# Kernel tuning notes

Measured on AMD Instinct MI355X. Metric: run time of the kernel, lower is better.

The kernel has to match this reference:

```python
import jax, jax.numpy as jnp
import numpy as np

N_NODES = 8192
N_EDGES = 65536
D_MODEL = 64
D_INNER = 128
D_STATE = 16
DT_RANK = 4
LAYER_NUM = 3
TAU = 0.01


def _unif(key, shape, fan_out):
    stdv = 1.0 / np.sqrt(fan_out)
    return jax.random.uniform(key, shape, jnp.float32, -stdv, stdv)


def setup_inputs() -> dict:
    key = jax.random.key(0)
    ks = jax.random.split(key, 12)
    x = jax.random.normal(ks[0], (N_NODES, D_MODEL), jnp.float32)
    edge_index = jax.random.randint(ks[1], (2, N_EDGES), 0, N_NODES, jnp.int64)
    in_proj_w = _unif(ks[2], (D_MODEL, 2 * D_INNER), 2 * D_INNER)
    x_proj_w = _unif(ks[3], (D_INNER, DT_RANK + 2 * D_STATE), DT_RANK + 2 * D_STATE)
    dt_proj_w = _unif(ks[4], (DT_RANK, D_INNER), D_INNER)
    out_proj_w = _unif(ks[5], (D_INNER, D_MODEL), D_MODEL)
    A_log = jnp.log(jnp.broadcast_to(jnp.arange(1, D_STATE + 1, dtype=jnp.float32)[None, :], (D_INNER, D_STATE)))
    D = jnp.ones((D_INNER,), jnp.float32)
    in_act_w = _unif(ks[6], (D_INNER, 2), 2)
    in_act_b = _unif(ks[7], (2,), 2)
    out_act_w = _unif(ks[8], (D_INNER, 2), 2)
    out_act_b = _unif(ks[9], (2,), 2)
    return {"x": x, "in_proj_w": in_proj_w, "x_proj_w": x_proj_w, "dt_proj_w": dt_proj_w,
            "A_log": A_log, "D": D, "out_proj_w": out_proj_w,
            "in_act_w": in_act_w, "in_act_b": in_act_b, "out_act_w": out_act_w, "out_act_b": out_act_b,
            "edge_index": edge_index, "layer_num": LAYER_NUM}


def _norm_adj(row, col, w, n_nodes):
    # SparseTensor(...).set_diag() adds diag value 1; symmetric deg^-1/2 renorm
    deg = jax.ops.segment_sum(w, row, num_segments=n_nodes) + 1.0
    dinv = jnp.where(deg > 0, deg ** -0.5, 0.0)
    return dinv[row] * w * dinv[col], dinv * dinv  # off-diag edge weights, diag weights


def _spmm(row, col, ew, dw, x, n_nodes):
    # adj @ x with adj = edges(ew) + diag(dw); x: [N, F]
    return jax.ops.segment_sum(ew[:, None] * x[col], row, num_segments=n_nodes) + dw[:, None] * x


def _gumbel_hard(logits, key, tau):
    g = jax.random.gumbel(key, logits.shape, logits.dtype)
    y = jax.nn.softmax((logits + g) / tau, axis=-1)
    hard = jax.nn.one_hot(jnp.argmax(y, axis=-1), logits.shape[-1], dtype=y.dtype)
    return hard + y - jax.lax.stop_gradient(y)


def reference(x, in_proj_w, x_proj_w, dt_proj_w, A_log, D, out_proj_w,
              in_act_w, in_act_b, out_act_w, out_act_b, edge_index, layer_num):
    n_nodes, d_model = x.shape
    d_inner = dt_proj_w.shape[1]
    n = A_log.shape[1]
    dt_rank = dt_proj_w.shape[0]
    row, col = edge_index[0], edge_index[1]

    xl = jnp.broadcast_to(x[:, None, :], (n_nodes, layer_num, d_model))  # [N,L,d_model]
    x_and_res = xl @ in_proj_w                                           # [N,L,2*d_inner]
    xs, res = jnp.split(x_and_res, 2, axis=-1)
    xs = jax.nn.relu(xs)                                                 # u in scan

    A = -jnp.exp(A_log)                                                  # [d_inner, n]
    x_dbl = xs @ x_proj_w                                                # [N,L,dt_rank+2n]
    delta = jax.nn.softplus(x_dbl[..., :dt_rank] @ dt_proj_w)            # [N,L,d_inner]
    B = x_dbl[..., dt_rank:dt_rank + n]                                  # [N,L,n]
    C = x_dbl[..., dt_rank + n:]                                         # [N,L,n]

    deltaA = jnp.exp(jnp.einsum('bld,dn->bldn', delta, A))               # [N,L,d_inner,n]
    deltaB_u = jnp.einsum('bld,bln->bldn', delta * xs, B)                # [N,L,d_inner,n]

    # initial adjacency: unit-weight edges, sym-normalized with self loops
    ew, dw = _norm_adj(row, col, jnp.ones((row.shape[0],), xs.dtype), n_nodes)
    state = jnp.zeros((n_nodes, d_inner, n), xs.dtype)
    gkey = jax.random.key(42)
    ys = []
    for i in range(layer_num):  # small fixed number of GCN/SSM steps
        state = deltaA[:, i] * state + deltaB_u[:, i]
        y = jnp.einsum('bdn,bn->bd', state, C[:, i])                     # [N,d_inner]
        flat = _spmm(row, col, ew, dw, state.reshape(n_nodes, d_inner * n), n_nodes)
        state = flat.reshape(n_nodes, d_inner, n)
        in_p = _gumbel_hard(y @ in_act_w + in_act_b, jax.random.fold_in(gkey, 2 * i), TAU)
        out_p = _gumbel_hard(y @ out_act_w + out_act_b, jax.random.fold_in(gkey, 2 * i + 1), TAU)
        w = in_p[col, 0] * out_p[row, 0]  # keep_in_prob[v] * keep_out_prob[u]
        ew, dw = _norm_adj(row, col, w, n_nodes)
        ys.append(y)

    y = jnp.stack(ys, axis=1) + xs * D                                   # [N,L,d_inner]
    y = y * jax.nn.relu(res)
    out = y @ out_proj_w                                                 # [N,L,d_model]
    return out[:, -1, :]
```

## Files before the change

kernel.cpp:

```cpp
#include <hip/hip_runtime.h>
#include <cstdint>

#define NN 8192
#define NE 65536
#define G 8
#define CAP 64

typedef _Float16 h8 __attribute__((ext_vector_type(8)));
typedef _Float16 h2 __attribute__((ext_vector_type(2)));

__device__ inline int rdlane_i(int v, int l) {
  return __builtin_amdgcn_readlane(v, l);
}
__device__ inline float rdlane_f(float v, int l) {
  return __int_as_float(__builtin_amdgcn_readlane(__float_as_int(v), l));
}

__host__ __device__ inline void tf2x32(uint32_t k0, uint32_t k1,
                                       uint32_t x0, uint32_t x1,
                                       uint32_t& r0, uint32_t& r1) {
  uint32_t ks2 = k0 ^ k1 ^ 0x1BD11BDAu;
  x0 += k0; x1 += k1;
#define TF_ROT(x,d) (((x)<<(d))|((x)>>(32-(d))))
#define TF_R4(ra,rb,rc,rd) \
  x0+=x1; x1=TF_ROT(x1,ra); x1^=x0; \
  x0+=x1; x1=TF_ROT(x1,rb); x1^=x0; \
  x0+=x1; x1=TF_ROT(x1,rc); x1^=x0; \
  x0+=x1; x1=TF_ROT(x1,rd); x1^=x0;
  TF_R4(13,15,26,6)  x0+=k1;  x1+=ks2+1u;
  TF_R4(17,29,16,24) x0+=ks2; x1+=k0+2u;
  TF_R4(13,15,26,6)  x0+=k0;  x1+=k1+3u;
  TF_R4(17,29,16,24) x0+=k1;  x1+=ks2+4u;
  TF_R4(13,15,26,6)  x0+=ks2; x1+=k0+5u;
  r0=x0; r1=x1;
#undef TF_R4
#undef TF_ROT
}

__device__ inline float gumbel32(uint32_t k0, uint32_t k1, uint32_t idx) {
  uint32_t a, b;
  tf2x32(k0, k1, 0u, idx, a, b);
  uint32_t bits = a ^ b;
  float f = __uint_as_float((bits >> 9) | 0x3f800000u) - 1.0f;
  float u = (f > 0.0f) ? f : 1.17549435e-38f;
  return -logf(-logf(u));
}

__global__ __launch_bounds__(256) void k_nodeprep(
    const float* __restrict__ x, const float* __restrict__ ipw,
    const float* __restrict__ xpw, const float* __restrict__ dtw,
    const float* __restrict__ iaw, const float* __restrict__ iab,
    const float* __restrict__ oaw, const float* __restrict__ oab,
    const float* __restrict__ alog, const float* __restrict__ wout,
    const int* __restrict__ ei,
    uint32_t ki0, uint32_t ki1, uint32_t ko0, uint32_t ko1,
    float* __restrict__ xs, float* __restrict__ rres,
    float* __restrict__ delta, _Float16* __restrict__ dxh2,
    float* __restrict__ Bm, float* __restrict__ Cm,
    float* __restrict__ inp, float* __restrict__ outp,
    float* __restrict__ Amat, _Float16* __restrict__ woT,
    int* __restrict__ cnt, int* __restrict__ csr_col) {
  __shared__ float sxs[G][128];
  __shared__ float sdbl[G][36];
  __shared__ float sdx[G][128];
  int t = threadIdx.x;
  int b0 = blockIdx.x * G;
  if (t < 64) {
    int e = blockIdx.x * 64 + t;
    int v = ei[e];
    int pos = atomicAdd(&cnt[v], 1);
    if (pos < CAP) csr_col[(v<<6) + pos] = ei[NE + e];
  }
  {
    int i = blockIdx.x * 8 + (t & 7);
    if (t < 8) {
      int d = i >> 6, oc = i & 63;
      woT[oc*128 + d] = (_Float16)wout[i];
    }
  }
  if (blockIdx.x == 0) {
    for (int i = t; i < 2048; i += 256) Amat[i] = -expf(alog[i]);
  }
  float acc[G];
#pragma unroll
  for (int g = 0; g < G; g++) acc[g] = 0.f;
  const float4* xb = (const float4*)(x + (size_t)b0 * 64);
  for (int k4 = 0; k4 < 16; k4++) {
    float w0 = ipw[(k4*4+0)*256 + t];
    float w1 = ipw[(k4*4+1)*256 + t];
    float w2 = ipw[(k4*4+2)*256 + t];
    float w3 = ipw[(k4*4+3)*256 + t];
#pragma unroll
    for (int g = 0; g < G; g++) {
      float4 xv = xb[g*16 + k4];
      acc[g] += xv.x*w0; acc[g] += xv.y*w1; acc[g] += xv.z*w2; acc[g] += xv.w*w3;
    }
  }
  if (t < 128) {
#pragma unroll
    for (int g = 0; g < G; g++) {
      float v = fmaxf(acc[g], 0.f);
      sxs[g][t] = v;
      xs[(size_t)(b0+g)*128 + t] = v;
    }
  } else {
    int j = t - 128;
#pragma unroll
    for (int g = 0; g < G; g++) rres[(size_t)(b0+g)*128 + j] = fmaxf(acc[g], 0.f);
  }
  __syncthreads();
  for (int idx = t; idx < G*36; idx += 256) {
    int g = idx / 36, c = idx % 36;
    float a = 0.f;
    for (int d4 = 0; d4 < 32; d4++) {
      float4 sv = ((const float4*)&sxs[g][0])[d4];
      a += sv.x*xpw[(d4*4+0)*36 + c];
      a += sv.y*xpw[(d4*4+1)*36 + c];
      a += sv.z*xpw[(d4*4+2)*36 + c];
      a += sv.w*xpw[(d4*4+3)*36 + c];
    }
    sdbl[g][c] = a;
    if (c >= 4 && c < 20)  Bm[(b0+g)*16 + (c-4)]  = a;
    else if (c >= 20)      Cm[(b0+g)*16 + (c-20)] = a;
  }
  __syncthreads();
  {
    int d = t & 127, hi = t >> 7;
#pragma unroll
    for (int gg = 0; gg < G/2; gg++) {
      int g = hi*(G/2) + gg;
      int b = b0 + g;
      float dt = sdbl[g][0]*dtw[d]     + sdbl[g][1]*dtw[128+d]
               + sdbl[g][2]*dtw[256+d] + sdbl[g][3]*dtw[384+d];
      float dv = fmaxf(dt, 0.f) + log1pf(expf(-fabsf(dt)));
      delta[(size_t)b*128 + d] = dv;
      sdx[g][d] = dv * sxs[g][d];
    }
  }
  __syncthreads();
  for (int i = t; i < G*64; i += 256) {
    int g = i >> 6, d = i & 63;
    h2 pk;
    pk.x = (_Float16)sdx[g][d];
    pk.y = (_Float16)sdx[g][d + 64];
    ((h2*)(dxh2 + ((size_t)(b0+g) << 7)))[d] = pk;
  }
  int wid = t >> 6, lane = t & 63;
#pragma unroll
  for (int s = 0; s < 2; s++) {
    int g = wid*2 + s;
    int b = b0 + g;
    float da = sdx[g][lane], db = sdx[g][lane + 64];
    float4 pr;
    pr.x = da*iaw[2*lane]   + db*iaw[2*(lane+64)];
    pr.y = da*iaw[2*lane+1] + db*iaw[2*(lane+64)+1];
    pr.z = da*oaw[2*lane]   + db*oaw[2*(lane+64)];
    pr.w = da*oaw[2*lane+1] + db*oaw[2*(lane+64)+1];
    for (int off = 32; off >= 1; off >>= 1) {
      pr.x += __shfl_down(pr.x, off);
      pr.y += __shfl_down(pr.y, off);
      pr.z += __shfl_down(pr.z, off);
      pr.w += __shfl_down(pr.w, off);
    }
    float gsel = 0.f;
    if (lane < 4) {
      uint32_t kk0 = (lane < 2) ? ki0 : ko0;
      uint32_t kk1 = (lane < 2) ? ki1 : ko1;
      gsel = gumbel32(kk0, kk1, 2u*(uint32_t)b + (uint32_t)(lane & 1));
    }
    float g0 = __shfl(gsel, 0), g1 = __shfl(gsel, 1);
    float g2 = __shfl(gsel, 2), g3 = __shfl(gsel, 3);
    if (lane == 0) {
      float BC = 0.f;
      for (int n = 0; n < 16; n++) BC += sdbl[g][4+n] * sdbl[g][20+n];
      float li0 = BC*pr.x + iab[0], li1 = BC*pr.y + iab[1];
      float lo0 = BC*pr.z + oab[0], lo1 = BC*pr.w + oab[1];
      inp[b]  = (li0 + g0 >= li1 + g1) ? 1.0f : 0.0f;
      outp[b] = (lo0 + g2 >= lo1 + g3) ? 1.0f : 0.0f;
    }
  }
}

__global__ __launch_bounds__(256) void k_spmm0f(
    const int* __restrict__ cnt, const int* __restrict__ csr_col,
    const float* __restrict__ inp, const float* __restrict__ outp,
    const float* __restrict__ delta, const _Float16* __restrict__ dxh2,
    const float* __restrict__ Bm, const float* __restrict__ Cm,
    const float* __restrict__ Amat,
    _Float16* __restrict__ s_out, float* __restrict__ dinv1,
    float* __restrict__ y2p) {
  int t = threadIdx.x, wid = t >> 6, lane = t & 63;
  int v = (blockIdx.x << 2) + wid;
  int deg = min(cnt[v], CAP);
  int   creg = 0;
  float cfreg = 0.f, gl = 0.f;
  if (lane < deg) {
    creg = csr_col[(v << 6) + lane];
    cfreg = 1.0f / sqrtf((float)min(cnt[creg], CAP) + 1.0f);
    gl = inp[creg];
  }
  float degs = gl;
#pragma unroll
  for (int off = 32; off >= 1; off >>= 1) degs += __shfl_xor(degs, off);
  int d0 = lane, d1 = lane + 64;
  float dv = 1.0f / sqrtf((float)deg + 1.0f);
  h2 pkv = ((const h2*)(dxh2 + ((size_t)v << 7)))[d0];
  float dx0 = (float)pkv.x, dx1 = (float)pkv.y;
  float Bf[16];
  {
    const float4* p = (const float4*)(Bm + ((size_t)v << 4));
    float4 q0 = p[0], q1 = p[1], q2 = p[2], q3 = p[3];
    Bf[0]=q0.x; Bf[1]=q0.y; Bf[2]=q0.z; Bf[3]=q0.w;
    Bf[4]=q1.x; Bf[5]=q1.y; Bf[6]=q1.z; Bf[7]=q1.w;
    Bf[8]=q2.x; Bf[9]=q2.y; Bf[10]=q2.z; Bf[11]=q2.w;
    Bf[12]=q3.x; Bf[13]=q3.y; Bf[14]=q3.z; Bf[15]=q3.w;
  }
  float a0[16], a1[16];
  {
    float dw = dv * dv;
    float c0 = dw * dx0, c1 = dw * dx1;
#pragma unroll
    for (int n = 0; n < 16; n++) { a0[n] = c0*Bf[n]; a1[n] = c1*Bf[n]; }
  }
#pragma unroll 2
  for (int j = 0; j < deg; j++) {
    int   c  = rdlane_i(creg, j);
    float cf = rdlane_f(cfreg, j);
    float coef = dv * cf;
    h2 pk = ((const h2*)(dxh2 + ((size_t)c << 7)))[d0];
    const float4* bp = (const float4*)(Bm + ((size_t)c << 4));
    float4 B0 = bp[0], B1 = bp[1], B2 = bp[2], B3 = bp[3];
    float e0 = coef * (float)pk.x;
    float e1 = coef * (float)pk.y;
    a0[0]+=e0*B0.x; a0[1]+=e0*B0.y; a0[2]+=e0*B0.z; a0[3]+=e0*B0.w;
    a0[4]+=e0*B1.x; a0[5]+=e0*B1.y; a0[6]+=e0*B1.z; a0[7]+=e0*B1.w;
    a0[8]+=e0*B2.x; a0[9]+=e0*B2.y; a0[10]+=e0*B2.z; a0[11]+=e0*B2.w;
    a0[12]+=e0*B3.x; a0[13]+=e0*B3.y; a0[14]+=e0*B3.z; a0[15]+=e0*B3.w;
    a1[0]+=e1*B0.x; a1[1]+=e1*B0.y; a1[2]+=e1*B0.z; a1[3]+=e1*B0.w;
    a1[4]+=e1*B1.x; a1[5]+=e1*B1.y; a1[6]+=e1*B1.z; a1[7]+=e1*B1.w;
    a1[8]+=e1*B2.x; a1[9]+=e1*B2.y; a1[10]+=e1*B2.z; a1[11]+=e1*B2.w;
    a1[12]+=e1*B3.x; a1[13]+=e1*B3.y; a1[14]+=e1*B3.z; a1[15]+=e1*B3.w;
  }
  float de0 = delta[(size_t)v*128 + d0], de1 = delta[(size_t)v*128 + d1];
  const float4* A0p = (const float4*)(Amat + (d0 << 4));
  const float4* A1p = (const float4*)(Amat + (d1 << 4));
  const float4* Cp  = (const float4*)(Cm + ((size_t)v << 4));
  float d1v = 1.0f / sqrtf(outp[v]*degs + 1.0f);
  if (lane == 0) dinv1[v] = d1v;
  float dw1 = d1v * d1v;
  float y0 = 0.f, y1 = 0.f, BvC = 0.f;
  _Float16 sh0[16], sh1[16];
#pragma unroll
  for (int q = 0; q < 4; q++) {
    float4 Aq0 = A0p[q], Aq1 = A1p[q], Cq = Cp[q];
    float A0a[4] = {Aq0.x, Aq0.y, Aq0.z, Aq0.w};
    float A1a[4] = {Aq1.x, Aq1.y, Aq1.z, Aq1.w};
    float Ca[4]  = {Cq.x, Cq.y, Cq.z, Cq.w};
#pragma unroll
    for (int i = 0; i < 4; i++) {
      int n = 4*q + i;
      float E0 = expf(de0 * A0a[i]);
      float E1 = expf(de1 * A1a[i]);
      float s0 = E0*a0[n] + dx0*Bf[n];
      float s1 = E1*a1[n] + dx1*Bf[n];
      y0 += E0*s0*Ca[i];
      y1 += E1*s1*Ca[i];
      BvC += Bf[n]*Ca[i];
      sh0[n] = (_Float16)s0;
      sh1[n] = (_Float16)s1;
    }
  }
  y0 = dw1*y0 + dx0*BvC;
  y1 = dw1*y1 + dx1*BvC;
  if (inp[v] != 0.f) {
    h8 P00, P01, P10, P11;
#pragma unroll
    for (int i = 0; i < 8; i++) {
      P00[i] = sh0[i]; P01[i] = sh0[8+i];
      P10[i] = sh1[i]; P11[i] = sh1[8+i];
    }
    h8* op = (h8*)(s_out + ((size_t)v << 11));
    op[2*lane]           = P00;
    op[2*lane + 1]       = P01;
    op[128 + 2*lane]     = P10;
    op[128 + 2*lane + 1] = P11;
  }
  y2p[(size_t)v*128 + d0] = y0;
  y2p[(size_t)v*128 + d1] = y1;
}

__global__ __launch_bounds__(256) void k_spmm1fo(
    const int* __restrict__ cnt, const int* __restrict__ csr_col,
    const float* __restrict__ dinv1,
    const float* __restrict__ inp, const float* __restrict__ outp,
    const float* __restrict__ delta,
    const float* __restrict__ Cm, const float* __restrict__ Amat,
    const _Float16* __restrict__ s_in, const float* __restrict__ y2p,
    const float* __restrict__ xs, const float* __restrict__ rres,
    const float* __restrict__ Dv, const _Float16* __restrict__ woT,
    float* __restrict__ out) {
  __shared__ float ty[4][128];
  int t = threadIdx.x, wid = t >> 6, lane = t & 63;
  int v = (blockIdx.x << 2) + wid;
  int deg = (outp[v] != 0.f) ? min(cnt[v], CAP) : 0;
  int   creg = 0;
  float cfreg = 0.f;
  if (lane < deg) {
    creg = csr_col[(v << 6) + lane];
    float g = inp[creg];
    cfreg = (g != 0.f) ? dinv1[creg] : 0.f;
  }
  unsigned long long mask = __ballot(cfreg != 0.f);
  int d0 = lane, d1 = lane + 64;
  float y0 = 0.f, y1 = 0.f;
  if (mask != 0ull) {
    float dv = dinv1[v];
    float a0[16], a1[16];
#pragma unroll
    for (int n = 0; n < 16; n++) { a0[n] = 0.f; a1[n] = 0.f; }
#pragma unroll 2
    for (int j = 0; j < deg; j++) {
      float cf = rdlane_f(cfreg, j);
      if (cf == 0.f) continue;
      int c = rdlane_i(creg, j);
      float coef = dv * cf;
      const h8* rp = (const h8*)(s_in + ((size_t)c << 11));
      h8 n00 = rp[2*lane], n01 = rp[2*lane+1];
      h8 n10 = rp[128 + 2*lane], n11 = rp[128 + 2*lane+1];
      a0[0]+=coef*(float)n00[0]; a0[1]+=coef*(float)n00[1];
      a0[2]+=coef*(float)n00[2]; a0[3]+=coef*(float)n00[3];
      a0[4]+=coef*(float)n00[4]; a0[5]+=coef*(float)n00[5];
      a0[6]+=coef*(float)n00[6]; a0[7]+=coef*(float)n00[7];
      a0[8]+=coef*(float)n01[0]; a0[9]+=coef*(float)n01[1];
      a0[10]+=coef*(float)n01[2]; a0[11]+=coef*(float)n01[3];
      a0[12]+=coef*(float)n01[4]; a0[13]+=coef*(float)n01[5];
      a0[14]+=coef*(float)n01[6]; a0[15]+=coef*(float)n01[7];
      a1[0]+=coef*(float)n10[0]; a1[1]+=coef*(float)n10[1];
      a1[2]+=coef*(float)n10[2]; a1[3]+=coef*(float)n10[3];
      a1[4]+=coef*(float)n10[4]; a1[5]+=coef*(float)n10[5];
      a1[6]+=coef*(float)n10[6]; a1[7]+=coef*(float)n10[7];
      a1[8]+=coef*(float)n11[0]; a1[9]+=coef*(float)n11[1];
      a1[10]+=coef*(float)n11[2]; a1[11]+=coef*(float)n11[3];
      a1[12]+=coef*(float)n11[4]; a1[13]+=coef*(float)n11[5];
      a1[14]+=coef*(float)n11[6]; a1[15]+=coef*(float)n11[7];
    }
    float de0 = delta[(size_t)v*128 + d0], de1 = delta[(size_t)v*128 + d1];
    const float4* A0p = (const float4*)(Amat + (d0 << 4));
    const float4* A1p = (const float4*)(Amat + (d1 << 4));
    const float4* Cp  = (const float4*)(Cm + ((size_t)v << 4));
#pragma unroll
    for (int q = 0; q < 4; q++) {
      float4 Aq0 = A0p[q], Aq1 = A1p[q], Cq = Cp[q];
      float A0a[4] = {Aq0.x, Aq0.y, Aq0.z, Aq0.w};
      float A1a[4] = {Aq1.x, Aq1.y, Aq1.z, Aq1.w};
      float Ca[4]  = {Cq.x, Cq.y, Cq.z, Cq.w};
#pragma unroll
      for (int i = 0; i < 4; i++) {
        int n = 4*q + i;
        y0 += expf(de0*A0a[i]) * a0[n] * Ca[i];
        y1 += expf(de1*A1a[i]) * a1[n] * Ca[i];
      }
    }
  }
  float t0 = (y0 + y2p[(size_t)v*128 + d0] + xs[(size_t)v*128 + d0]*Dv[d0]) * rres[(size_t)v*128 + d0];
  float t1 = (y1 + y2p[(size_t)v*128 + d1] + xs[(size_t)v*128 + d1]*Dv[d1]) * rres[(size_t)v*128 + d1];
  ty[wid][d0] = t0;
  ty[wid][d1] = t1;
  asm volatile("s_waitcnt lgkmcnt(0)" ::: "memory");
  __builtin_amdgcn_sched_barrier(0);
  float acc = 0.f;
  const float4* tyv = (const float4*)&ty[wid][0];
  const h8* wrow = (const h8*)(woT + ((size_t)lane << 7));
#pragma unroll
  for (int ch = 0; ch < 16; ch++) {
    h8 wv = wrow[ch];
    float4 u0 = tyv[2*ch], u1 = tyv[2*ch+1];
    acc += u0.x*(float)wv[0] + u0.y*(float)wv[1] + u0.z*(float)wv[2] + u0.w*(float)wv[3]
         + u1.x*(float)wv[4] + u1.y*(float)wv[5] + u1.z*(float)wv[6] + u1.w*(float)wv[7];
  }
  out[(size_t)v*64 + lane] = acc;
}

extern "C" void kernel_launch(void* const* d_in, const int* in_sizes, int n_in,
                              void* d_out, int out_size, void* d_ws, size_t ws_size,
                              hipStream_t stream) {
  const float* x    = (const float*)d_in[0];
  const float* ipw  = (const float*)d_in[1];
  const float* xpw  = (const float*)d_in[2];
  const float* dtw  = (const float*)d_in[3];
  const float* alog = (const float*)d_in[4];
  const float* Dv   = (const float*)d_in[5];
  const float* wout = (const float*)d_in[6];
  const float* iaw  = (const float*)d_in[7];
  const float* iab  = (const float*)d_in[8];
  const float* oaw  = (const float*)d_in[9];
  const float* oab  = (const float*)d_in[10];
  const int*   ei   = (const int*)d_in[11];
  (void)in_sizes; (void)n_in; (void)out_size; (void)ws_size;

  float* W = (float*)d_ws;
  size_t o = 0;
  float* xs    = W + o; o += (size_t)NN*128;
  float* rres  = W + o; o += (size_t)NN*128;
  float* delta = W + o; o += (size_t)NN*128;
  float* y2p   = W + o; o += (size_t)NN*128;
  float* Bm    = W + o; o += (size_t)NN*16;
  float* Cm    = W + o; o += (size_t)NN*16;
  float* Amat  = W + o; o += 2048;
  float* dinv1 = W + o; o += NN;
  float* inp   = W + o; o += NN;
  float* outp  = W + o; o += NN;
  _Float16* dxh2 = (_Float16*)(W + o); o += (size_t)NN*64;
  o += (size_t)NN*8;
  _Float16* woT  = (_Float16*)(W + o); o += 4096;
  _Float16* stA  = (_Float16*)(W + o); o += (size_t)NN*1024;
  int* cnt     = (int*)(W + o);
  int* csr_col = cnt + NN;

  uint32_t ki0, ki1, ko0, ko1;
  tf2x32(0u, 42u, 0u, 0u, ki0, ki1);
  tf2x32(0u, 42u, 0u, 1u, ko0, ko1);

  hipMemsetAsync(cnt, 0, NN*sizeof(int), stream);

  k_nodeprep<<<NN/G, 256, 0, stream>>>(x, ipw, xpw, dtw, iaw, iab, oaw, oab,
                                       alog, wout, ei, ki0, ki1, ko0, ko1,
                                       xs, rres, delta, dxh2, Bm, Cm,
                                       inp, outp, Amat, woT, cnt, csr_col);

  k_spmm0f<<<NN/4, 256, 0, stream>>>(cnt, csr_col, inp, outp,
                                     delta, dxh2, Bm, Cm, Amat,
                                     stA, dinv1, y2p);

  k_spmm1fo<<<NN/4, 256, 0, stream>>>(cnt, csr_col, dinv1, inp, outp,
                                      delta, Cm, Amat, stA, y2p,
                                      xs, rres, Dv, woT, (float*)d_out);
}
```

Before: 160.3 us.

## Split each node's d_inner channels across two waves in both SpMM kernels

Both SpMM kernels now assign one node to two waves, each wave handling 64 of the 128 inner channels, instead of one wave covering all 128. This halves the per-thread accumulator registers and doubles the number of waves, which is meant to raise occupancy and latency hiding for the gather-bound loops. The output projection is split by channel halves and combined through shared memory with block-wide barriers. The cost is duplicated neighbour-list loads, reductions and B-row reads per node, plus the added synchronisation.

```diff
diff --git a/kernel.cpp b/kernel.cpp
--- a/kernel.cpp
+++ b/kernel.cpp
@@ -189,9 +189,13 @@
     const float* __restrict__ Amat,
     _Float16* __restrict__ s_out, float* __restrict__ dinv1,
     float* __restrict__ y2p) {
-  int t = threadIdx.x, wid = t >> 6, lane = t & 63;
-  int v = (blockIdx.x << 2) + wid;
+  int t = threadIdx.x, wave = t >> 6, lane = t & 63;
+  int v = (blockIdx.x << 1) + (wave >> 1);
+  int w = wave & 1;
+  int d = (w << 6) + lane;
   int deg = min(cnt[v], CAP);
+  float inpv = inp[v];
+  float outpv = outp[v];
   int   creg = 0;
   float cfreg = 0.f, gl = 0.f;
   if (lane < deg) {
@@ -202,10 +206,9 @@
   float degs = gl;
 #pragma unroll
   for (int off = 32; off >= 1; off >>= 1) degs += __shfl_xor(degs, off);
-  int d0 = lane, d1 = lane + 64;
   float dv = 1.0f / sqrtf((float)deg + 1.0f);
-  h2 pkv = ((const h2*)(dxh2 + ((size_t)v << 7)))[d0];
-  float dx0 = (float)pkv.x, dx1 = (float)pkv.y;
+  h2 pkv = ((const h2*)(dxh2 + ((size_t)v << 7)))[lane];
+  float dx = w ? (float)pkv.y : (float)pkv.x;
   float Bf[16];
   {
     const float4* p = (const float4*)(Bm + ((size_t)v << 4));
@@ -215,78 +218,59 @@
     Bf[8]=q2.x; Bf[9]=q2.y; Bf[10]=q2.z; Bf[11]=q2.w;
     Bf[12]=q3.x; Bf[13]=q3.y; Bf[14]=q3.z; Bf[15]=q3.w;
   }
-  float a0[16], a1[16];
+  float a[16];
   {
-    float dw = dv * dv;
-    float c0 = dw * dx0, c1 = dw * dx1;
-#pragma unroll
-    for (int n = 0; n < 16; n++) { a0[n] = c0*Bf[n]; a1[n] = c1*Bf[n]; }
-  }
-#pragma unroll 2
+    float c0 = dv * dv * dx;
+#pragma unroll
+    for (int n = 0; n < 16; n++) a[n] = c0*Bf[n];
+  }
+#pragma unroll 4
   for (int j = 0; j < deg; j++) {
     int   c  = rdlane_i(creg, j);
     float cf = rdlane_f(cfreg, j);
     float coef = dv * cf;
-    h2 pk = ((const h2*)(dxh2 + ((size_t)c << 7)))[d0];
+    h2 pk = ((const h2*)(dxh2 + ((size_t)c << 7)))[lane];
     const float4* bp = (const float4*)(Bm + ((size_t)c << 4));
     float4 B0 = bp[0], B1 = bp[1], B2 = bp[2], B3 = bp[3];
-    float e0 = coef * (float)pk.x;
-    float e1 = coef * (float)pk.y;
-    a0[0]+=e0*B0.x; a0[1]+=e0*B0.y; a0[2]+=e0*B0.z; a0[3]+=e0*B0.w;
-    a0[4]+=e0*B1.x; a0[5]+=e0*B1.y; a0[6]+=e0*B1.z; a0[7]+=e0*B1.w;
-    a0[8]+=e0*B2.x; a0[9]+=e0*B2.y; a0[10]+=e0*B2.z; a0[11]+=e0*B2.w;
-    a0[12]+=e0*B3.x; a0[13]+=e0*B3.y; a0[14]+=e0*B3.z; a0[15]+=e0*B3.w;
-    a1[0]+=e1*B0.x; a1[1]+=e1*B0.y; a1[2]+=e1*B0.z; a1[3]+=e1*B0.w;
-    a1[4]+=e1*B1.x; a1[5]+=e1*B1.y; a1[6]+=e1*B1.z; a1[7]+=e1*B1.w;
-    a1[8]+=e1*B2.x; a1[9]+=e1*B2.y; a1[10]+=e1*B2.z; a1[11]+=e1*B2.w;
-    a1[12]+=e1*B3.x; a1[13]+=e1*B3.y; a1[14]+=e1*B3.z; a1[15]+=e1*B3.w;
-  }
-  float de0 = delta[(size_t)v*128 + d0], de1 = delta[(size_t)v*128 + d1];
-  const float4* A0p = (const float4*)(Amat + (d0 << 4));
-  const float4* A1p = (const float4*)(Amat + (d1 << 4));
-  const float4* Cp  = (const float4*)(Cm + ((size_t)v << 4));
-  float d1v = 1.0f / sqrtf(outp[v]*degs + 1.0f);
-  if (lane == 0) dinv1[v] = d1v;
+    float e = coef * (w ? (float)pk.y : (float)pk.x);
+    a[0]+=e*B0.x; a[1]+=e*B0.y; a[2]+=e*B0.z; a[3]+=e*B0.w;
+    a[4]+=e*B1.x; a[5]+=e*B1.y; a[6]+=e*B1.z; a[7]+=e*B1.w;
+    a[8]+=e*B2.x; a[9]+=e*B2.y; a[10]+=e*B2.z; a[11]+=e*B2.w;
+    a[12]+=e*B3.x; a[13]+=e*B3.y; a[14]+=e*B3.z; a[15]+=e*B3.w;
+  }
+  float de = delta[(size_t)v*128 + d];
+  const float4* Ap = (const float4*)(Amat + (d << 4));
+  const float4* Cp = (const float4*)(Cm + ((size_t)v << 4));
+  float d1v = 1.0f / sqrtf(outpv*degs + 1.0f);
+  if (w == 0 && lane == 0) dinv1[v] = d1v;
   float dw1 = d1v * d1v;
-  float y0 = 0.f, y1 = 0.f, BvC = 0.f;
-  _Float16 sh0[16], sh1[16];
+  float y = 0.f, BvC = 0.f;
+  _Float16 sh[16];
 #pragma unroll
   for (int q = 0; q < 4; q++) {
-    float4 Aq0 = A0p[q], Aq1 = A1p[q], Cq = Cp[q];
-    float A0a[4] = {Aq0.x, Aq0.y, Aq0.z, Aq0.w};
-    float A1a[4] = {Aq1.x, Aq1.y, Aq1.z, Aq1.w};
-    float Ca[4]  = {Cq.x, Cq.y, Cq.z, Cq.w};
+    float4 Aq = Ap[q], Cq = Cp[q];
+    float Aa[4] = {Aq.x, Aq.y, Aq.z, Aq.w};
+    float Ca[4] = {Cq.x, Cq.y, Cq.z, Cq.w};
 #pragma unroll
     for (int i = 0; i < 4; i++) {
       int n = 4*q + i;
-      float E0 = expf(de0 * A0a[i]);
-      float E1 = expf(de1 * A1a[i]);
-      float s0 = E0*a0[n] + dx0*Bf[n];
-      float s1 = E1*a1[n] + dx1*Bf[n];
-      y0 += E0*s0*Ca[i];
-      y1 += E1*s1*Ca[i];
+      float E = expf(de * Aa[i]);
+      float s = E*a[n] + dx*Bf[n];
+      y += E*s*Ca[i];
       BvC += Bf[n]*Ca[i];
-      sh0[n] = (_Float16)s0;
-      sh1[n] = (_Float16)s1;
-    }
-  }
-  y0 = dw1*y0 + dx0*BvC;
-  y1 = dw1*y1 + dx1*BvC;
-  if (inp[v] != 0.f) {
-    h8 P00, P01, P10, P11;
-#pragma unroll
-    for (int i = 0; i < 8; i++) {
-      P00[i] = sh0[i]; P01[i] = sh0[8+i];
-      P10[i] = sh1[i]; P11[i] = sh1[8+i];
-    }
+      sh[n] = (_Float16)s;
+    }
+  }
+  y = dw1*y + dx*BvC;
+  if (inpv != 0.f) {
+    h8 P0, P1;
+#pragma unroll
+    for (int i = 0; i < 8; i++) { P0[i] = sh[i]; P1[i] = sh[8+i]; }
     h8* op = (h8*)(s_out + ((size_t)v << 11));
-    op[2*lane]           = P00;
-    op[2*lane + 1]       = P01;
-    op[128 + 2*lane]     = P10;
-    op[128 + 2*lane + 1] = P11;
-  }
-  y2p[(size_t)v*128 + d0] = y0;
-  y2p[(size_t)v*128 + d1] = y1;
+    op[(w ? 128 : 0) + 2*lane]     = P0;
+    op[(w ? 128 : 0) + 2*lane + 1] = P1;
+  }
+  y2p[(size_t)v*128 + d] = y;
 }
 
 __global__ __launch_bounds__(256) void k_spmm1fo(
@@ -299,9 +283,13 @@
     const float* __restrict__ xs, const float* __restrict__ rres,
     const float* __restrict__ Dv, const _Float16* __restrict__ woT,
     float* __restrict__ out) {
-  __shared__ float ty[4][128];
-  int t = threadIdx.x, wid = t >> 6, lane = t & 63;
-  int v = (blockIdx.x << 2) + wid;
+  __shared__ float sty[2][128];
+  __shared__ float sproj[2][64];
+  int t = threadIdx.x, wave = t >> 6, lane = t & 63;
+  int nd = wave >> 1;
+  int v = (blockIdx.x << 1) + nd;
+  int w = wave & 1;
+  int d = (w << 6) + lane;
   int deg = (outp[v] != 0.f) ? min(cnt[v], CAP) : 0;
   int   creg = 0;
   float cfreg = 0.f;
@@ -311,74 +299,62 @@
     cfreg = (g != 0.f) ? dinv1[creg] : 0.f;
   }
   unsigned long long mask = __ballot(cfreg != 0.f);
-  int d0 = lane, d1 = lane + 64;
-  float y0 = 0.f, y1 = 0.f;
+  float y = 0.f;
   if (mask != 0ull) {
-    float dv = dinv1[v];
-    float a0[16], a1[16];
-#pragma unroll
-    for (int n = 0; n < 16; n++) { a0[n] = 0.f; a1[n] = 0.f; }
-#pragma unroll 2
+    float dvv = dinv1[v];
+    float a[16];
+#pragma unroll
+    for (int n = 0; n < 16; n++) a[n] = 0.f;
+#pragma unroll 4
     for (int j = 0; j < deg; j++) {
       float cf = rdlane_f(cfreg, j);
       if (cf == 0.f) continue;
       int c = rdlane_i(creg, j);
-      float coef = dv * cf;
+      float coef = dvv * cf;
       const h8* rp = (const h8*)(s_in + ((size_t)c << 11));
-      h8 n00 = rp[2*lane], n01 = rp[2*lane+1];
-      h8 n10 = rp[128 + 2*lane], n11 = rp[128 + 2*lane+1];
-      a0[0]+=coef*(float)n00[0]; a0[1]+=coef*(float)n00[1];
-      a0[2]+=coef*(float)n00[2]; a0[3]+=coef*(float)n00[3];
-      a0[4]+=coef*(float)n00[4]; a0[5]+=coef*(float)n00[5];
-      a0[6]+=coef*(float)n00[6]; a0[7]+=coef*(float)n00[7];
-      a0[8]+=coef*(float)n01[0]; a0[9]+=coef*(float)n01[1];
-      a0[10]+=coef*(float)n01[2]; a0[11]+=coef*(float)n01[3];
-      a0[12]+=coef*(float)n01[4]; a0[13]+=coef*(float)n01[5];
-      a0[14]+=coef*(float)n01[6]; a0[15]+=coef*(float)n01[7];
-      a1[0]+=coef*(float)n10[0]; a1[1]+=coef*(float)n10[1];
-      a1[2]+=coef*(float)n10[2]; a1[3]+=coef*(float)n10[3];
-      a1[4]+=coef*(float)n10[4]; a1[5]+=coef*(float)n10[5];
-      a1[6]+=coef*(float)n10[6]; a1[7]+=coef*(float)n10[7];
-      a1[8]+=coef*(float)n11[0]; a1[9]+=coef*(float)n11[1];
-      a1[10]+=coef*(float)n11[2]; a1[11]+=coef*(float)n11[3];
-      a1[12]+=coef*(float)n11[4]; a1[13]+=coef*(float)n11[5];
-      a1[14]+=coef*(float)n11[6]; a1[15]+=coef*(float)n11[7];
-    }
-    float de0 = delta[(size_t)v*128 + d0], de1 = delta[(size_t)v*128 + d1];
-    const float4* A0p = (const float4*)(Amat + (d0 << 4));
-    const float4* A1p = (const float4*)(Amat + (d1 << 4));
-    const float4* Cp  = (const float4*)(Cm + ((size_t)v << 4));
+      h8 n0 = rp[(w ? 128 : 0) + 2*lane];
+      h8 n1 = rp[(w ? 128 : 0) + 2*lane + 1];
+      a[0]+=coef*(float)n0[0]; a[1]+=coef*(float)n0[1];
+      a[2]+=coef*(float)n0[2]; a[3]+=coef*(float)n0[3];
+      a[4]+=coef*(float)n0[4]; a[5]+=coef*(float)n0[5];
+      a[6]+=coef*(float)n0[6]; a[7]+=coef*(float)n0[7];
+      a[8]+=coef*(float)n1[0]; a[9]+=coef*(float)n1[1];
+      a[10]+=coef*(float)n1[2]; a[11]+=coef*(float)n1[3];
+      a[12]+=coef*(float)n1[4]; a[13]+=coef*(float)n1[5];
+      a[14]+=coef*(float)n1[6]; a[15]+=coef*(float)n1[7];
+    }
+    float de = delta[(size_t)v*128 + d];
+    const float4* Ap = (const float4*)(Amat + (d << 4));
+    const float4* Cp = (const float4*)(Cm + ((size_t)v << 4));
 #pragma unroll
     for (int q = 0; q < 4; q++) {
-      float4 Aq0 = A0p[q], Aq1 = A1p[q], Cq = Cp[q];
-      float A0a[4] = {Aq0.x, Aq0.y, Aq0.z, Aq0.w};
-      float A1a[4] = {Aq1.x, Aq1.y, Aq1.z, Aq1.w};
-      float Ca[4]  = {Cq.x, Cq.y, Cq.z, Cq.w};
+      float4 Aq = Ap[q], Cq = Cp[q];
+      float Aa[4] = {Aq.x, Aq.y, Aq.z, Aq.w};
+      float Ca[4] = {Cq.x, Cq.y, Cq.z, Cq.w};
 #pragma unroll
       for (int i = 0; i < 4; i++) {
         int n = 4*q + i;
-        y0 += expf(de0*A0a[i]) * a0[n] * Ca[i];
-        y1 += expf(de1*A1a[i]) * a1[n] * Ca[i];
+        y += expf(de*Aa[i]) * a[n] * Ca[i];
       }
     }
   }
-  float t0 = (y0 + y2p[(size_t)v*128 + d0] + xs[(size_t)v*128 + d0]*Dv[d0]) * rres[(size_t)v*128 + d0];
-  float t1 = (y1 + y2p[(size_t)v*128 + d1] + xs[(size_t)v*128 + d1]*Dv[d1]) * rres[(size_t)v*128 + d1];
-  ty[wid][d0] = t0;
-  ty[wid][d1] = t1;
-  asm volatile("s_waitcnt lgkmcnt(0)" ::: "memory");
-  __builtin_amdgcn_sched_barrier(0);
+  float tv = (y + y2p[(size_t)v*128 + d] + xs[(size_t)v*128 + d]*Dv[d]) * rres[(size_t)v*128 + d];
+  sty[nd][d] = tv;
+  __syncthreads();
   float acc = 0.f;
-  const float4* tyv = (const float4*)&ty[wid][0];
+  const float4* tyv = (const float4*)&sty[nd][0];
   const h8* wrow = (const h8*)(woT + ((size_t)lane << 7));
 #pragma unroll
-  for (int ch = 0; ch < 16; ch++) {
+  for (int i = 0; i < 8; i++) {
+    int ch = (w << 3) + i;
     h8 wv = wrow[ch];
     float4 u0 = tyv[2*ch], u1 = tyv[2*ch+1];
     acc += u0.x*(float)wv[0] + u0.y*(float)wv[1] + u0.z*(float)wv[2] + u0.w*(float)wv[3]
          + u1.x*(float)wv[4] + u1.y*(float)wv[5] + u1.z*(float)wv[6] + u1.w*(float)wv[7];
   }
-  out[(size_t)v*64 + lane] = acc;
+  if (w == 1) sproj[nd][lane] = acc;
+  __syncthreads();
+  if (w == 0) out[(size_t)v*64 + lane] = acc + sproj[nd][lane];
 }
 
 extern "C" void kernel_launch(void* const* d_in, const int* in_sizes, int n_in,
@@ -428,11 +404,11 @@
                                        xs, rres, delta, dxh2, Bm, Cm,
                                        inp, outp, Amat, woT, cnt, csr_col);
 
-  k_spmm0f<<<NN/4, 256, 0, stream>>>(cnt, csr_col, inp, outp,
+  k_spmm0f<<<NN/2, 256, 0, stream>>>(cnt, csr_col, inp, outp,
                                      delta, dxh2, Bm, Cm, Amat,
                                      stA, dinv1, y2p);
 
-  k_spmm1fo<<<NN/4, 256, 0, stream>>>(cnt, csr_col, dinv1, inp, outp,
+  k_spmm1fo<<<NN/2, 256, 0, stream>>>(cnt, csr_col, dinv1, inp, outp,
                                       delta, Cm, Amat, stA, y2p,
                                       xs, rres, Dv, woT, (float*)d_out);
 }
```

Result: slower. 170.3 us (+6.2%).
